# Performance work log

Measured on AMD Instinct MI355X. Metric: run time of the kernel, lower is better.

Reference implementation:

```python
import jax, jax.numpy as jnp
import numpy as np

# module hyperparameters (init_kwargs)
SLEN = 208          # full image side length in pixels
PTILE = 8           # padded tile side length
STEP = 2            # tile stride
EDGE = 3            # edge padding; tile interior = PTILE - 2*EDGE = 2 = STEP
MAXDET = 2          # max detections kept per tile


def _tile_coords():
    # replicates _get_tile_coords: coords[i] = [i // ny * step, i % ny * step]
    n = (SLEN - PTILE) // STEP + 1
    i = np.arange(n * n)
    coords = np.stack([(i // n) * STEP, (i % n) * STEP], axis=1).astype(np.float32)
    return jnp.asarray(coords)  # (P, 2)


def setup_inputs() -> dict:
    key = jax.random.key(0)
    k1, k2 = jax.random.split(key)
    locs = jax.random.uniform(k1, (16, 100, 2), dtype=jnp.float32)    # in [0,1)
    fluxes = jax.random.uniform(k2, (16, 100, 5), dtype=jnp.float32)
    return {"locs": locs, "fluxes": fluxes}


def reference(locs, fluxes):
    # Faithful translation of _get_params_in_tiles(tile_coords, max_detections,
    # slen, edge_padding, ptile_slen, locs, fluxes).
    tc = _tile_coords()                     # (P, 2)
    B, S, _ = locs.shape
    P = tc.shape[0]

    locs_pix = locs * (SLEN - 1)            # (B, S, 2) pixel coords
    left = tc + EDGE - 0.5                  # (P, 2)
    right = tc - 0.5 + PTILE - EDGE         # (P, 2)

    lp = locs_pix[:, None, :, :]            # (B, 1, S, 2)
    on2 = (lp > left[None, :, None, :]) & (lp < right[None, :, None, :]) & (lp != 0.0)
    is_on = (on2[..., 0] & on2[..., 1]).astype(jnp.float32)   # (B, P, S)
    is_on_flat = is_on.reshape(B * P, S)
    tile_n_sources = is_on_flat.sum(axis=1).astype(jnp.int64) if False else is_on_flat.sum(axis=1).astype(jnp.int32)

    # masked per-tile locations, shifted to tile-local coords, scaled, relu'd
    scale = PTILE - 2 * EDGE
    tile_locs = is_on[..., None] * locs_pix[:, None, :, :]     # (B, P, S, 2)
    tile_locs = (tile_locs - left[None, :, None, :]) / scale
    tile_locs = jax.nn.relu(tile_locs).reshape(B * P, S, 2)

    # front-sort: on-entries first (jax argsort is stable)
    idx = jnp.argsort(-is_on_flat.astype(jnp.int32), axis=1)   # (B*P, S)
    tile_locs = jnp.take_along_axis(tile_locs, idx[..., None], axis=1)

    # masked + gathered per-tile params (fluxes)
    tile_fluxes = (is_on[..., None] * fluxes[:, None, :, :]).reshape(B * P, S, -1)
    tile_fluxes = jnp.take_along_axis(tile_fluxes, idx[..., None], axis=1)

    tile_is_on = jnp.take_along_axis(is_on_flat, idx, axis=1)  # (B*P, S)

    # clip to max_detections
    tile_n_sources = jnp.minimum(tile_n_sources, MAXDET)
    return (tile_n_sources,
            tile_locs[:, :MAXDET],
            tile_fluxes[:, :MAXDET],
            tile_is_on[:, :MAXDET])
```

## Files before the change

### kernel.cpp

```cpp
#include <hip/hip_runtime.h>

#define NT     101
#define PTILES (NT * NT)
#define BATCH  16
#define NSRC   100
#define NTILES (BATCH * PTILES)
#define PBLK   256
#define NBLKX  ((PTILES + PBLK - 1) / PBLK)


__global__ __launch_bounds__(256)
void ImageEncoder_41944650613092_kernel(const float* __restrict__ locs,
                                        const float* __restrict__ fluxes,
                                        float* __restrict__ out)
{
    __shared__ int   s_cnt[2];
    __shared__ int   s_tc[NSRC];
    __shared__ int   s_id[NSRC];
    __shared__ float s_y[NSRC];
    __shared__ float s_x[NSRC];
    __shared__ float s_f[PBLK * 10];

    const int tid   = threadIdx.x;
    const int b     = blockIdx.y;
    const int pbase = blockIdx.x * PBLK;
    const int p     = pbase + tid;

    bool  m  = false;
    int   tc = -1;
    float yp = 0.f, xp = 0.f;
    if (tid < NSRC) {
        const float2 yx = ((const float2*)(locs + b * (NSRC * 2)))[tid];
        yp = yx.x * 207.0f;
        xp = yx.y * 207.0f;
        int r = (int)floorf((yp - 2.5f) * 0.5f);
        int c = (int)floorf((xp - 2.5f) * 0.5f);
        bool ok = (r >= 0) & (r < NT) & (c >= 0) & (c < NT);
        if (ok) {
            const float ly = (float)(2 * r) + 2.5f;
            const float lx = (float)(2 * c) + 2.5f;
            ok = (yp > ly) & (yp < ly + 2.0f) & (xp > lx) & (xp < lx + 2.0f);
        }
        tc = r * NT + c;
        m  = ok & (tc >= pbase) & (tc < pbase + PBLK);
    }

    int pos = 0;
    if (tid < 128) {
        const unsigned long long ball = __ballot(m);
        const int lane = tid & 63;
        const int wave = tid >> 6;
        if (lane == 0) s_cnt[wave] = __popcll(ball);
        pos = __popcll(ball & ((1ull << lane) - 1ull));
    }
    __syncthreads();
    if (m) {
        const int idx = ((tid >> 6) ? s_cnt[0] : 0) + pos;
        s_tc[idx] = tc;
        s_id[idx] = tid;
        s_y[idx]  = yp;
        s_x[idx]  = xp;
    }
    const int total = s_cnt[0] + s_cnt[1];
    __syncthreads();

    int cnt = 0, i0 = -1, i1 = -1;
    for (int i = 0; i < total; ++i) {
        if (s_tc[i] == p) {
            if (cnt == 0)      i0 = i;
            else if (cnt == 1) i1 = i;
            ++cnt;
        }
    }

    float l4[4]   = {0.f, 0.f, 0.f, 0.f};
    float f10[10] = {0.f, 0.f, 0.f, 0.f, 0.f, 0.f, 0.f, 0.f, 0.f, 0.f};
    float o2[2]   = {0.f, 0.f};

    const int row = p / NT;
    const int col = p - row * NT;
    const float ly = (float)(2 * row) + 2.5f;
    const float lx = (float)(2 * col) + 2.5f;

    #pragma unroll
    for (int k = 0; k < 2; ++k) {
        const int i = (k == 0) ? i0 : i1;
        if (i >= 0) {
            l4[2 * k]     = (s_y[i] - ly) * 0.5f;
            l4[2 * k + 1] = (s_x[i] - lx) * 0.5f;
            const float* fb = fluxes + (size_t)(b * NSRC + s_id[i]) * 5;
            #pragma unroll
            for (int j = 0; j < 5; ++j) f10[5 * k + j] = fb[j];
            o2[k] = 1.0f;
        }
    }

    float* out_n = out;
    float* out_l = out + NTILES;
    float* out_f = out + (size_t)NTILES * 5;
    float* out_o = out + (size_t)NTILES * 15;

    const int t = b * PTILES + p;
    if (p < PTILES) {
        out_n[t] = fminf((float)cnt, 2.0f);
        *(float4*)(out_l + (size_t)t * 4) = make_float4(l4[0], l4[1], l4[2], l4[3]);
        *(float2*)(out_o + (size_t)t * 2) = make_float2(o2[0], o2[1]);
    }

    #pragma unroll
    for (int j = 0; j < 10; ++j) s_f[tid * 10 + j] = f10[j];
    __syncthreads();

    const int nvalid = min(PTILES - pbase, PBLK);
    const int nfl2   = nvalid * 5;
    float2* dst = (float2*)(out_f + ((size_t)b * PTILES + pbase) * 10);
    const float2* src = (const float2*)s_f;
    for (int i = tid; i < nfl2; i += PBLK) dst[i] = src[i];
}

extern "C" void kernel_launch(void* const* d_in, const int* in_sizes, int n_in,
                              void* d_out, int out_size, void* d_ws, size_t ws_size,
                              hipStream_t stream) {
    const float* locs   = (const float*)d_in[0];
    const float* fluxes = (const float*)d_in[1];
    float* out = (float*)d_out;

    dim3 grid(NBLKX, BATCH);
    ImageEncoder_41944650613092_kernel<<<grid, 256, 0, stream>>>(locs, fluxes, out);
}
```

Measured before the change: 58.91 us.

## Split into bulk zero-fill plus sparse per-source scatter kernel

Replaces the per-tile kernel, which scanned the source list for every tile and staged fluxes through shared memory, with two kernels. The first zero-fills the whole output with float4 stores. The second uses one block per batch and one thread per source: each source computes its rank among sources in the same tile and scatters its values directly. This removes the per-tile scan and shared staging, at the cost of an extra launch and scattered writes from only 16 small blocks.

```diff
diff --git a/kernel.cpp b/kernel.cpp
--- a/kernel.cpp
+++ b/kernel.cpp
@@ -5,32 +5,33 @@
 #define BATCH  16
 #define NSRC   100
 #define NTILES (BATCH * PTILES)
-#define PBLK   256
-#define NBLKX  ((PTILES + PBLK - 1) / PBLK)
-
+#define TOTF   (17 * NTILES)
+#define F4TOT  (TOTF / 4)
 
 __global__ __launch_bounds__(256)
-void ImageEncoder_41944650613092_kernel(const float* __restrict__ locs,
-                                        const float* __restrict__ fluxes,
-                                        float* __restrict__ out)
+void ImageEncoder_zero_fill(float4* __restrict__ out)
 {
-    __shared__ int   s_cnt[2];
-    __shared__ int   s_tc[NSRC];
-    __shared__ int   s_id[NSRC];
-    __shared__ float s_y[NSRC];
-    __shared__ float s_x[NSRC];
-    __shared__ float s_f[PBLK * 10];
+    const int stride = gridDim.x * blockDim.x;
+    for (int i = blockIdx.x * blockDim.x + threadIdx.x; i < F4TOT; i += stride)
+        out[i] = make_float4(0.f, 0.f, 0.f, 0.f);
+}
 
-    const int tid   = threadIdx.x;
-    const int b     = blockIdx.y;
-    const int pbase = blockIdx.x * PBLK;
-    const int p     = pbase + tid;
+__global__ __launch_bounds__(128)
+void ImageEncoder_sparse_fill(const float* __restrict__ locs,
+                              const float* __restrict__ fluxes,
+                              float* __restrict__ out)
+{
+    __shared__ int   s_tc[128];
+    __shared__ float s_y[128];
+    __shared__ float s_x[128];
 
-    bool  m  = false;
+    const int s = threadIdx.x;
+    const int b = blockIdx.x;
+
     int   tc = -1;
     float yp = 0.f, xp = 0.f;
-    if (tid < NSRC) {
-        const float2 yx = ((const float2*)(locs + b * (NSRC * 2)))[tid];
+    if (s < NSRC) {
+        const float2 yx = ((const float2*)(locs + b * (NSRC * 2)))[s];
         yp = yx.x * 207.0f;
         xp = yx.y * 207.0f;
         int r = (int)floorf((yp - 2.5f) * 0.5f);
@@ -41,58 +42,21 @@
             const float lx = (float)(2 * c) + 2.5f;
             ok = (yp > ly) & (yp < ly + 2.0f) & (xp > lx) & (xp < lx + 2.0f);
         }
-        tc = r * NT + c;
-        m  = ok & (tc >= pbase) & (tc < pbase + PBLK);
+        if (ok) tc = r * NT + c;
     }
-
-    int pos = 0;
-    if (tid < 128) {
-        const unsigned long long ball = __ballot(m);
-        const int lane = tid & 63;
-        const int wave = tid >> 6;
-        if (lane == 0) s_cnt[wave] = __popcll(ball);
-        pos = __popcll(ball & ((1ull << lane) - 1ull));
-    }
-    __syncthreads();
-    if (m) {
-        const int idx = ((tid >> 6) ? s_cnt[0] : 0) + pos;
-        s_tc[idx] = tc;
-        s_id[idx] = tid;
-        s_y[idx]  = yp;
-        s_x[idx]  = xp;
-    }
-    const int total = s_cnt[0] + s_cnt[1];
+    s_tc[s] = tc;
+    s_y[s]  = yp;
+    s_x[s]  = xp;
     __syncthreads();
 
-    int cnt = 0, i0 = -1, i1 = -1;
-    for (int i = 0; i < total; ++i) {
-        if (s_tc[i] == p) {
-            if (cnt == 0)      i0 = i;
-            else if (cnt == 1) i1 = i;
-            ++cnt;
-        }
-    }
+    if (tc < 0) return;
 
-    float l4[4]   = {0.f, 0.f, 0.f, 0.f};
-    float f10[10] = {0.f, 0.f, 0.f, 0.f, 0.f, 0.f, 0.f, 0.f, 0.f, 0.f};
-    float o2[2]   = {0.f, 0.f};
-
-    const int row = p / NT;
-    const int col = p - row * NT;
-    const float ly = (float)(2 * row) + 2.5f;
-    const float lx = (float)(2 * col) + 2.5f;
-
-    #pragma unroll
-    for (int k = 0; k < 2; ++k) {
-        const int i = (k == 0) ? i0 : i1;
-        if (i >= 0) {
-            l4[2 * k]     = (s_y[i] - ly) * 0.5f;
-            l4[2 * k + 1] = (s_x[i] - lx) * 0.5f;
-            const float* fb = fluxes + (size_t)(b * NSRC + s_id[i]) * 5;
-            #pragma unroll
-            for (int j = 0; j < 5; ++j) f10[5 * k + j] = fb[j];
-            o2[k] = 1.0f;
-        }
+    int rank = 0, cnt = 0;
+    #pragma unroll 4
+    for (int j = 0; j < NSRC; ++j) {
+        const bool same = (s_tc[j] == tc);
+        cnt  += same ? 1 : 0;
+        rank += (same & (j < s)) ? 1 : 0;
     }
 
     float* out_n = out;
@@ -100,22 +64,27 @@
     float* out_f = out + (size_t)NTILES * 5;
     float* out_o = out + (size_t)NTILES * 15;
 
-    const int t = b * PTILES + p;
-    if (p < PTILES) {
+    const int t = b * PTILES + tc;
+
+    if (rank == 0)
         out_n[t] = fminf((float)cnt, 2.0f);
-        *(float4*)(out_l + (size_t)t * 4) = make_float4(l4[0], l4[1], l4[2], l4[3]);
-        *(float2*)(out_o + (size_t)t * 2) = make_float2(o2[0], o2[1]);
+
+    if (rank < 2) {
+        const int   row = tc / NT;
+        const int   col = tc - row * NT;
+        const float ly  = (float)(2 * row) + 2.5f;
+        const float lx  = (float)(2 * col) + 2.5f;
+
+        *(float2*)(out_l + (size_t)t * 4 + 2 * rank) =
+            make_float2((yp - ly) * 0.5f, (xp - lx) * 0.5f);
+
+        out_o[(size_t)t * 2 + rank] = 1.0f;
+
+        const float* fb = fluxes + (size_t)(b * NSRC + s) * 5;
+        float*       fo = out_f + (size_t)t * 10 + 5 * rank;
+        #pragma unroll
+        for (int j = 0; j < 5; ++j) fo[j] = fb[j];
     }
-
-    #pragma unroll
-    for (int j = 0; j < 10; ++j) s_f[tid * 10 + j] = f10[j];
-    __syncthreads();
-
-    const int nvalid = min(PTILES - pbase, PBLK);
-    const int nfl2   = nvalid * 5;
-    float2* dst = (float2*)(out_f + ((size_t)b * PTILES + pbase) * 10);
-    const float2* src = (const float2*)s_f;
-    for (int i = tid; i < nfl2; i += PBLK) dst[i] = src[i];
 }
 
 extern "C" void kernel_launch(void* const* d_in, const int* in_sizes, int n_in,
@@ -125,6 +94,7 @@
     const float* fluxes = (const float*)d_in[1];
     float* out = (float*)d_out;
 
-    dim3 grid(NBLKX, BATCH);
-    ImageEncoder_41944650613092_kernel<<<grid, 256, 0, stream>>>(locs, fluxes, out);
+    ImageEncoder_zero_fill<<<dim3(678), 256, 0, stream>>>((float4*)out);
+
+    ImageEncoder_sparse_fill<<<dim3(BATCH), 128, 0, stream>>>(locs, fluxes, out);
 }
```

After: 63.15 us. 7.2% more time.
